# Kernel optimization log

Measured on AMD Instinct MI355X. Metric: run time of the kernel, lower is better.

The kernel has to match this reference:

```python
import jax, jax.numpy as jnp
import numpy as np

C = 128      # hidden_channels
H = 4        # heads
DH = C // H
G = 4096     # num genes (segments)
R = 4096     # num reactions
E = 65536    # total (reaction, gene) pairs
LMAX = 64    # padded segment length
NB = 4       # blocks: 2 encoder SABs + 1 PMA + 1 decoder SAB
EPS = 1e-5


def _ln(x, g, b):
    m = jnp.mean(x, axis=-1, keepdims=True)
    v = jnp.mean((x - m) ** 2, axis=-1, keepdims=True)
    return (x - m) * jax.lax.rsqrt(v + EPS) * g + b


def setup_inputs() -> dict:
    key = jax.random.key(0)
    ks = jax.random.split(key, 12)
    sc = 1.0 / np.sqrt(C)
    zb = jnp.zeros((NB, C), jnp.float32)
    ob = jnp.ones((NB, C), jnp.float32)
    # every gene gets >= 1 reaction (matches realistic GEM mapping; avoids empty segments)
    gene_idx = jnp.sort(jnp.concatenate([
        jnp.arange(G, dtype=jnp.int32),
        jax.random.randint(ks[8], (E - G,), 0, G, jnp.int32)]))
    return {
        'reaction_features': jax.random.normal(ks[0], (R, C), jnp.float32),
        'Wq': jax.random.normal(ks[1], (NB, C, C), jnp.float32) * sc,
        'Wk': jax.random.normal(ks[2], (NB, C, C), jnp.float32) * sc,
        'Wv': jax.random.normal(ks[3], (NB, C, C), jnp.float32) * sc,
        'Wo': jax.random.normal(ks[4], (NB, C, C), jnp.float32) * sc,
        'bq': zb, 'bk': zb, 'bv': zb, 'bo': zb,
        'Wlin': jax.random.normal(ks[5], (NB, C, C), jnp.float32) * sc,
        'blin': zb,
        'g1': ob, 'b1': zb, 'g2': ob, 'b2': zb,
        'seed': jax.random.normal(ks[6], (1, 1, C), jnp.float32) * sc,
        'rxn_idx': jax.random.randint(ks[7], (E,), 0, R, jnp.int32),
        'gene_idx': gene_idx,
        'num_genes': G,
        'Lmax': LMAX,
    }


def _forward(reaction_features, Wq, Wk, Wv, Wo, bq, bk, bv, bo, Wlin, blin,
             g1, b1, g2, b2, seed, rxn_idx, gene_idx, num_genes, Lmax):
    E_ = gene_idx.shape[0]
    feats = reaction_features[rxn_idx]                      # [E, C] gather
    counts = jax.ops.segment_sum(jnp.ones((E_,), jnp.int32), gene_idx,
                                 num_segments=num_genes)
    starts = jnp.cumsum(counts) - counts                    # first flat index of each segment
    pos = jnp.arange(E_, dtype=jnp.int32) - starts[gene_idx]
    # to_dense_batch: [G, Lmax, C] + mask
    x = jnp.zeros((num_genes, Lmax, C), feats.dtype).at[gene_idx, pos].set(feats, mode='drop')
    mask = jnp.zeros((num_genes, Lmax), bool).at[gene_idx, pos].set(True, mode='drop')

    def mab(q_in, kv_in, q_mask, kv_mask, i):
        B, Lq, _ = q_in.shape
        Lk = kv_in.shape[1]
        q = (q_in @ Wq[i] + bq[i]).reshape(B, Lq, H, DH)
        k = (kv_in @ Wk[i] + bk[i]).reshape(B, Lk, H, DH)
        v = (kv_in @ Wv[i] + bv[i]).reshape(B, Lk, H, DH)
        scores = jnp.einsum('bqhd,bkhd->bhqk', q, k) / np.sqrt(DH)
        if kv_mask is not None:
            scores = jnp.where(kv_mask[:, None, None, :], scores, -1e30)
        a = jax.nn.softmax(scores, axis=-1)
        attn = jnp.einsum('bhqk,bkhd->bqhd', a, v).reshape(B, Lq, C) @ Wo[i] + bo[i]
        if q_mask is not None:
            attn = jnp.where(q_mask[:, :, None], attn, 0.0)
        out = _ln(attn + q_in, g1[i], b1[i])
        out = out + jax.nn.relu(out @ Wlin[i] + blin[i])
        return _ln(out, g2[i], b2[i])

    h = mab(x, x, mask, mask, 0)          # encoder SAB 1
    h = mab(h, h, mask, mask, 1)          # encoder SAB 2
    s = jnp.broadcast_to(seed, (num_genes, seed.shape[1], C))
    h = mab(s, h, None, mask, 2)          # PMA (1 seed point)
    h = mab(h, h, None, None, 3)          # decoder SAB
    h = jnp.nan_to_num(h)
    return h.reshape(num_genes, -1)       # [G, C] (concat over 1 seed)


def reference(reaction_features, Wq, Wk, Wv, Wo, bq, bk, bv, bo, Wlin, blin,
              g1, b1, g2, b2, seed, rxn_idx, gene_idx, num_genes, Lmax):
    return _forward(reaction_features, Wq, Wk, Wv, Wo, bq, bk, bv, bo, Wlin,
                    blin, g1, b1, g2, b2, seed, rxn_idx, gene_idx, num_genes, Lmax)
```

## Files before the change

### kernel.cpp

```cpp
#include <hip/hip_runtime.h>
#include <hip/hip_bf16.h>
#include <math.h>

#define C 128
#define H 4
#define LMAX 64
#define EPS 1e-5f
#define ISQ 0.17677669529663687f

using short8  = __attribute__((ext_vector_type(8))) short;
using short4v = __attribute__((ext_vector_type(4))) short;
using f32x4   = __attribute__((ext_vector_type(4))) float;

__device__ __forceinline__ float wsum(float v){
  #pragma unroll
  for (int o = 32; o > 0; o >>= 1) v += __shfl_xor(v, o, 64);
  return v;
}
__device__ __forceinline__ float wmax(float v){
  #pragma unroll
  for (int o = 32; o > 0; o >>= 1) v = fmaxf(v, __shfl_xor(v, o, 64));
  return v;
}
__device__ __forceinline__ short f2bs(float f){
  __hip_bfloat16 b = __float2bfloat16(f);
  union { __hip_bfloat16 b; short u; } cv; cv.b = b; return cv.u;
}
__device__ __forceinline__ float b2f(short u){
  return __uint_as_float(((unsigned)(unsigned short)u) << 16);
}

__global__ void prep_wfrag(const float* __restrict__ Wq, const float* __restrict__ Wk,
                           const float* __restrict__ Wv, const float* __restrict__ Wo,
                           const float* __restrict__ Wlin, short* __restrict__ wf){
  int bid = blockIdx.x, l = threadIdx.x;
  int tile = bid & 31, mb = bid >> 5;
  int mat = mb >> 2, blk = mb & 3;
  const float* W = (mat==0?Wq : mat==1?Wk : mat==2?Wv : mat==3?Wo : Wlin) + blk*C*C;
  int nt = tile >> 2, kt = tile & 3;
  int col = nt*16 + (l & 15);
  int k0  = kt*32 + ((l >> 4) << 3);
  short8 v;
  #pragma unroll
  for (int j = 0; j < 8; j++) v[j] = f2bs(W[(k0 + j)*C + col]);
  *(short8*)(wf + ((size_t)mb*32 + tile)*512 + (size_t)l*8) = v;
}

__global__ void prep_qrow(const float* __restrict__ seed, const float* __restrict__ Wq,
                          const float* __restrict__ bq, float* __restrict__ qrow){
  int t = threadIdx.x;
  const float* wq2 = Wq + 2*C*C;
  float acc = bq[2*C + t];
  #pragma unroll 4
  for (int k = 0; k < C; k++) acc = fmaf(seed[k], wq2[k*C + t], acc);
  qrow[t] = acc;
}

__global__ void seg_kernel(const int* __restrict__ gidx, int E, int G,
                           int* __restrict__ starts, int* __restrict__ counts,
                           int* __restrict__ cnt, int* __restrict__ gcr){
  int g = blockIdx.x * blockDim.x + threadIdx.x;
  if (g >= G) return;
  int lo = 0, hi = E;
  while (lo < hi){ int m = (lo + hi) >> 1; if (gidx[m] < g) lo = m + 1; else hi = m; }
  int s = lo; hi = E;
  while (lo < hi){ int m = (lo + hi) >> 1; if (gidx[m] < g + 1) lo = m + 1; else hi = m; }
  starts[g] = s;
  int c_ = lo - s; counts[g] = c_;
  int L = c_ > LMAX ? LMAX : c_; if (L < 1) L = 1;
  int cl = (L - 1) >> 4;
  int r = atomicAdd(&cnt[cl], 1);
  gcr[g] = (cl << 28) | r;
}

__global__ void fill_kernel(int G, const int* __restrict__ cnt, const int* __restrict__ gcr,
                            int* __restrict__ binfo, int* __restrict__ nbins){
  int g = blockIdx.x * blockDim.x + threadIdx.x;
  if (g >= G) return;
  int nb1 = (cnt[0] + 3) >> 2, nb2 = (cnt[1] + 1) >> 1, nb3 = cnt[2];
  if (g == 0) *nbins = nb1 + nb2 + nb3 + cnt[3];
  int v = gcr[g]; int cl = v >> 28; int r = v & 0x0FFFFFFF;
  int bin, slot;
  if      (cl == 0){ bin = r >> 2;             slot = r & 3; }
  else if (cl == 1){ bin = nb1 + (r >> 1);     slot = (r & 1) * 2; }
  else if (cl == 2){ bin = nb1 + nb2 + r;      slot = 0; }
  else             { bin = nb1 + nb2 + nb3 + r; slot = 0; }
  binfo[bin*4 + slot] = g;
}

__device__ __forceinline__ f32x4 mfma4(short8 a0, short8 a1, short8 a2, short8 a3,
                                       const short* __restrict__ wf, int nt, int l){
  f32x4 acc = {0.f, 0.f, 0.f, 0.f};
  acc = __builtin_amdgcn_mfma_f32_16x16x32_bf16(a0, *(const short8*)(wf + ((nt*4+0)*64 + l)*8), acc, 0,0,0);
  acc = __builtin_amdgcn_mfma_f32_16x16x32_bf16(a1, *(const short8*)(wf + ((nt*4+1)*64 + l)*8), acc, 0,0,0);
  acc = __builtin_amdgcn_mfma_f32_16x16x32_bf16(a2, *(const short8*)(wf + ((nt*4+2)*64 + l)*8), acc, 0,0,0);
  acc = __builtin_amdgcn_mfma_f32_16x16x32_bf16(a3, *(const short8*)(wf + ((nt*4+3)*64 + l)*8), acc, 0,0,0);
  return acc;
}

__device__ __forceinline__ void ln_rows(const short (*src)[136], short (*dst)[136],
                                        const float* __restrict__ gg,
                                        const float* __restrict__ bb, int t){
  int row = t >> 2, q4 = t & 3;
  float v[32];
  float sm = 0.f;
  #pragma unroll
  for (int kk = 0; kk < 32; ++kk){
    float x = b2f(src[row][q4*32 + kk]);
    v[kk] = x; sm += x;
  }
  sm += __shfl_xor(sm, 1);
  sm += __shfl_xor(sm, 2);
  float mean = sm * (1.f/128.f);
  float s2 = 0.f;
  #pragma unroll
  for (int kk = 0; kk < 32; ++kk){ float d = v[kk] - mean; s2 += d*d; }
  s2 += __shfl_xor(s2, 1);
  s2 += __shfl_xor(s2, 2);
  float rs = rsqrtf(s2*(1.f/128.f) + EPS);
  #pragma unroll
  for (int kk = 0; kk < 32; ++kk){
    int col = q4*32 + kk;
    dst[row][col] = f2bs((v[kk] - mean)*rs*gg[col] + bb[col]);
  }
}

__global__ __launch_bounds__(256, 2) void gene_bin_kernel(
  const float* __restrict__ RF, const short* __restrict__ wfrag,
  const float* __restrict__ qrow,
  const float* __restrict__ bq, const float* __restrict__ bk,
  const float* __restrict__ bv, const float* __restrict__ bo,
  const float* __restrict__ blin,
  const float* __restrict__ g1, const float* __restrict__ b1,
  const float* __restrict__ g2, const float* __restrict__ b2,
  const int* __restrict__ rxn_idx, const int* __restrict__ starts,
  const int* __restrict__ counts, const int* __restrict__ binfo,
  const int* __restrict__ meta, float* __restrict__ pooled)
{
  if ((int)blockIdx.x >= meta[0]) return;
  __shared__ short xb[64][136];
  __shared__ short qb[64][136];
  __shared__ short kb[64][136];
  __shared__ short vt[128][72];
  __shared__ __align__(16) short sc[64][72];
  __shared__ float qrl[C];
  __shared__ int mg[4], mL[4], ms0[4], mbase[4];

  const int bin = blockIdx.x;
  const int t = threadIdx.x, w = t >> 6, l = t & 63;
  const int hi = l >> 4, c = l & 15;

  if (t == 0){
    int s = 0;
    while (s < 4){
      int g = binfo[bin*4 + s];
      if (g >= 0){
        int Lg = counts[g]; if (Lg > LMAX) Lg = LMAX;
        int ntg = (Lg + 15) >> 4;
        for (int u = 0; u < ntg; ++u){ mg[s+u] = g; mL[s+u] = Lg; ms0[s+u] = starts[g]; mbase[s+u] = s; }
        s += ntg;
      } else { mg[s] = -1; mL[s] = 0; ms0[s] = 0; mbase[s] = s; s++; }
    }
  }
  if (t < C) qrl[t] = qrow[t];
  __syncthreads();

  for (int idx = t; idx < 64*16; idx += 256){
    int row = idx >> 4, ch = idx & 15;
    int s = row >> 4;
    int g = mg[s];
    int ro = row - mbase[s]*16;
    short8 u = {0,0,0,0,0,0,0,0};
    if (g >= 0 && ro < mL[s]){
      int rr = rxn_idx[ms0[s] + ro];
      const float* src = RF + (size_t)rr*C + ch*8;
      float4 v0 = *(const float4*)(src);
      float4 v1 = *(const float4*)(src + 4);
      u[0]=f2bs(v0.x); u[1]=f2bs(v0.y); u[2]=f2bs(v0.z); u[3]=f2bs(v0.w);
      u[4]=f2bs(v1.x); u[5]=f2bs(v1.y); u[6]=f2bs(v1.z); u[7]=f2bs(v1.w);
    }
    *(short8*)&xb[row][ch*8] = u;
  }
  {
    short8 z = {0,0,0,0,0,0,0,0};
    for (int idx = t; idx < 64*9; idx += 256){
      int row = idx / 9, ch = idx - row*9;
      *(short8*)&sc[row][ch*8] = z;
    }
  }
  __syncthreads();

  const int myg = mg[w];

  for (int blk = 0; blk < 2; ++blk){
    {
      short8 ax[4][4];
      #pragma unroll
      for (int mt = 0; mt < 4; ++mt)
        #pragma unroll
        for (int kk = 0; kk < 4; ++kk)
          ax[mt][kk] = *(const short8*)&xb[mt*16 + c][kk*32 + hi*8];
      #pragma unroll
      for (int i = 0; i < 6; ++i){
        int pr = w + 4*i;
        int mat = pr >> 3, nt = pr & 7;
        const short* wfm = wfrag + (size_t)(mat*4 + blk)*16384;
        const float* bias = (mat == 0 ? bq : mat == 1 ? bk : bv);
        int col = nt*16 + c;
        float bb = bias[blk*C + col];
        #pragma unroll
        for (int mt = 0; mt < 4; ++mt){
          f32x4 acc = mfma4(ax[mt][0], ax[mt][1], ax[mt][2], ax[mt][3], wfm, nt, l);
          if (mat == 2){
            short4v pk;
            #pragma unroll
            for (int r = 0; r < 4; r++) pk[r] = f2bs(acc[r] + bb);
            *(short4v*)&vt[col][mt*16 + hi*4] = pk;
          } else if (mat == 0){
            #pragma unroll
            for (int r = 0; r < 4; r++) qb[mt*16 + hi*4 + r][col] = f2bs(acc[r] + bb);
          } else {
            #pragma unroll
            for (int r = 0; r < 4; r++) kb[mt*16 + hi*4 + r][col] = f2bs(acc[r] + bb);
          }
        }
      }
    }
    __syncthreads();

    for (int h = 0; h < H; ++h){
      if (myg >= 0){
        short8 a = *(const short8*)&qb[w*16 + c][h*32 + hi*8];
        #pragma unroll
        for (int kt = 0; kt < 4; ++kt){
          if (mg[kt] == myg){
            short8 b = *(const short8*)&kb[kt*16 + c][h*32 + hi*8];
            f32x4 acc = {0.f, 0.f, 0.f, 0.f};
            acc = __builtin_amdgcn_mfma_f32_16x16x32_bf16(a, b, acc, 0,0,0);
            #pragma unroll
            for (int r = 0; r < 4; r++) sc[w*16 + hi*4 + r][kt*16 + c] = f2bs(acc[r] * ISQ);
          }
        }
      }
      {
        int row = t >> 2, q4 = t & 3;
        int s = row >> 4;
        if (mg[s] >= 0){
          int kbeg = mbase[s]*16;
          int kend = kbeg + mL[s];
          int send = kbeg + (((mL[s] + 15) >> 4) << 4);
          int b0 = q4*16;
          float e[16];
          float mx = -3.4e38f;
          #pragma unroll
          for (int kk = 0; kk < 16; ++kk){
            int col = b0 + kk;
            bool ok = (col >= kbeg) && (col < kend);
            float lg = ok ? b2f(sc[row][col]) : -3.4e38f;
            e[kk] = lg;
            mx = fmaxf(mx, lg);
          }
          mx = fmaxf(mx, __shfl_xor(mx, 1));
          mx = fmaxf(mx, __shfl_xor(mx, 2));
          float sm = 0.f;
          #pragma unroll
          for (int kk = 0; kk < 16; ++kk){
            int col = b0 + kk;
            bool ok = (col >= kbeg) && (col < kend);
            float ee = ok ? __expf(e[kk] - mx) : 0.f;
            e[kk] = ee; sm += ee;
          }
          sm += __shfl_xor(sm, 1);
          sm += __shfl_xor(sm, 2);
          float inv = 1.f / sm;
          #pragma unroll
          for (int kk = 0; kk < 16; ++kk){
            int col = b0 + kk;
            if (col >= kbeg && col < send)
              sc[row][col] = f2bs((col < kend) ? e[kk]*inv : 0.f);
          }
        }
      }
      if (myg >= 0){
        #pragma unroll
        for (int dt = 0; dt < 2; ++dt){
          f32x4 acc = {0.f, 0.f, 0.f, 0.f};
          #pragma unroll
          for (int ks = 0; ks < 2; ++ks){
            short8 a = *(const short8*)&sc[w*16 + c][ks*32 + hi*8];
            short8 b = *(const short8*)&vt[h*32 + dt*16 + c][ks*32 + hi*8];
            acc = __builtin_amdgcn_mfma_f32_16x16x32_bf16(a, b, acc, 0,0,0);
          }
          int col = h*32 + dt*16 + c;
          #pragma unroll
          for (int r = 0; r < 4; r++) qb[w*16 + hi*4 + r][col] = f2bs(acc[r]);
        }
      }
    }
    __syncthreads();

    {
      short8 aq[4][4];
      #pragma unroll
      for (int mt = 0; mt < 4; ++mt)
        #pragma unroll
        for (int kk = 0; kk < 4; ++kk)
          aq[mt][kk] = *(const short8*)&qb[mt*16 + c][kk*32 + hi*8];
      const short* wfo = wfrag + (size_t)(3*4 + blk)*16384;
      #pragma unroll
      for (int i = 0; i < 2; ++i){
        int nt = w + 4*i;
        int col = nt*16 + c;
        float bb = bo[blk*C + col];
        #pragma unroll
        for (int mt = 0; mt < 4; ++mt){
          f32x4 acc = mfma4(aq[mt][0], aq[mt][1], aq[mt][2], aq[mt][3], wfo, nt, l);
          #pragma unroll
          for (int r = 0; r < 4; r++){
            int row = mt*16 + hi*4 + r;
            xb[row][col] = f2bs(acc[r] + bb + b2f(xb[row][col]));
          }
        }
      }
    }
    __syncthreads();
    ln_rows(xb, xb, g1 + blk*C, b1 + blk*C, t);
    __syncthreads();

    {
      short8 af[4][4];
      #pragma unroll
      for (int mt = 0; mt < 4; ++mt)
        #pragma unroll
        for (int kk = 0; kk < 4; ++kk)
          af[mt][kk] = *(const short8*)&xb[mt*16 + c][kk*32 + hi*8];
      const short* wfl = wfrag + (size_t)(4*4 + blk)*16384;
      #pragma unroll
      for (int i = 0; i < 2; ++i){
        int nt = w + 4*i;
        int col = nt*16 + c;
        float bb = blin[blk*C + col];
        #pragma unroll
        for (int mt = 0; mt < 4; ++mt){
          f32x4 acc = mfma4(af[mt][0], af[mt][1], af[mt][2], af[mt][3], wfl, nt, l);
          #pragma unroll
          for (int r = 0; r < 4; r++){
            int row = mt*16 + hi*4 + r;
            kb[row][col] = f2bs(b2f(xb[row][col]) + fmaxf(acc[r] + bb, 0.f));
          }
        }
      }
    }
    __syncthreads();
    ln_rows(kb, xb, g2 + blk*C, b2 + blk*C, t);
    __syncthreads();
  }

  {
    short8 ap[4][4];
    #pragma unroll
    for (int mt = 0; mt < 4; ++mt)
      #pragma unroll
      for (int kk = 0; kk < 4; ++kk)
        ap[mt][kk] = *(const short8*)&xb[mt*16 + c][kk*32 + hi*8];
    const short* wfk2 = wfrag + (size_t)(1*4 + 2)*16384;
    const short* wfv2 = wfrag + (size_t)(2*4 + 2)*16384;
    #pragma unroll
    for (int i = 0; i < 4; ++i){
      int pr = w + 4*i;
      int mat = pr >> 3, nt = pr & 7;
      const short* wfm = mat ? wfv2 : wfk2;
      const float* bias = mat ? bv : bk;
      int col = nt*16 + c;
      float bb = bias[2*C + col];
      #pragma unroll
      for (int mt = 0; mt < 4; ++mt){
        f32x4 acc = mfma4(ap[mt][0], ap[mt][1], ap[mt][2], ap[mt][3], wfm, nt, l);
        if (!mat){
          #pragma unroll
          for (int r = 0; r < 4; r++) kb[mt*16 + hi*4 + r][col] = f2bs(acc[r] + bb);
        } else {
          short4v pk;
          #pragma unroll
          for (int r = 0; r < 4; r++) pk[r] = f2bs(acc[r] + bb);
          *(short4v*)&vt[col][mt*16 + hi*4] = pk;
        }
      }
    }
  }
  __syncthreads();
  {
    int g = mg[w];
    if (g >= 0 && mbase[w] == w){
      int L = mL[w];
      int row = w*16 + l;
      float* ps = (float*)&sc[0][0];
      #pragma unroll
      for (int h = 0; h < 4; ++h){
        float a = -3.4e38f;
        if (l < L){
          float acc = 0.f;
          #pragma unroll 8
          for (int dd = 0; dd < 32; ++dd)
            acc = fmaf(b2f(kb[row][h*32 + dd]), qrl[h*32 + dd], acc);
          a = acc * ISQ;
        }
        float mx = wmax(a);
        float e = (l < L) ? __expf(a - mx) : 0.f;
        float s = wsum(e);
        ps[(w*4 + h)*64 + l] = e / s;
      }
      #pragma unroll
      for (int half = 0; half < 2; ++half){
        int d = l + half*64;
        int h = d >> 5;
        float acc = 0.f;
        for (int kk = 0; kk < L; ++kk)
          acc = fmaf(ps[(w*4 + h)*64 + kk], b2f(vt[d][w*16 + kk]), acc);
        pooled[(size_t)g*C + d] = acc;
      }
    }
  }
}

__device__ __forceinline__ void gemmf(const float (*src)[132], const float* __restrict__ W,
                                      float (&o)[4], int col, int rg){
  #pragma unroll
  for (int r = 0; r < 4; ++r) o[r] = 0.f;
  #pragma unroll 8
  for (int k = 0; k < 128; ++k){
    float wv = W[k*C + col];
    #pragma unroll
    for (int r = 0; r < 4; ++r) o[r] = fmaf(src[rg*4 + r][k], wv, o[r]);
  }
}

__device__ __forceinline__ void ln16f(float (*buf)[132], const float* __restrict__ gg,
                                      const float* __restrict__ bb, int t){
  int row = t >> 4, cg = t & 15;
  float v[8]; float s = 0.f;
  #pragma unroll
  for (int k = 0; k < 8; ++k){ v[k] = buf[row][cg*8 + k]; s += v[k]; }
  s += __shfl_xor(s,1); s += __shfl_xor(s,2); s += __shfl_xor(s,4); s += __shfl_xor(s,8);
  float mean = s * (1.f/128.f);
  float q = 0.f;
  #pragma unroll
  for (int k = 0; k < 8; ++k){ float d = v[k] - mean; q += d*d; }
  q += __shfl_xor(q,1); q += __shfl_xor(q,2); q += __shfl_xor(q,4); q += __shfl_xor(q,8);
  float rs = rsqrtf(q*(1.f/128.f) + EPS);
  #pragma unroll
  for (int k = 0; k < 8; ++k)
    buf[row][cg*8 + k] = (v[k] - mean)*rs*gg[cg*8 + k] + bb[cg*8 + k];
}

__global__ __launch_bounds__(512) void tail_kernel(
  const float* __restrict__ pooled,
  const float* __restrict__ Wv, const float* __restrict__ Wo,
  const float* __restrict__ Wlin,
  const float* __restrict__ bv, const float* __restrict__ bo,
  const float* __restrict__ blin,
  const float* __restrict__ g1, const float* __restrict__ b1,
  const float* __restrict__ g2, const float* __restrict__ b2,
  const float* __restrict__ seed, float* __restrict__ out, int G)
{
  __shared__ float ta[16][132];
  __shared__ float tb[16][132];
  const int t = threadIdx.x;
  const int g0 = blockIdx.x * 16;
  const int col = t & 127, rg = t >> 7;
  float o[4], res[4];

  if (t < 256){
    int row = t >> 4, ch = t & 15;
    float4 v0 = {0,0,0,0}, v1 = {0,0,0,0};
    if (g0 + row < G){
      const float* src = pooled + (size_t)(g0 + row)*C + ch*8;
      v0 = *(const float4*)(src);
      v1 = *(const float4*)(src + 4);
    }
    *(float4*)&ta[row][ch*8] = v0;
    *(float4*)&ta[row][ch*8 + 4] = v1;
  }
  __syncthreads();

  gemmf(ta, Wo + 2*C*C, o, col, rg);
  {
    float ss = seed[col], bb = bo[2*C + col];
    #pragma unroll
    for (int r = 0; r < 4; ++r) tb[rg*4 + r][col] = o[r] + bb + ss;
  }
  __syncthreads();
  if (t < 256) ln16f(tb, g1 + 2*C, b1 + 2*C, t);
  __syncthreads();
  gemmf(tb, Wlin + 2*C*C, o, col, rg);
  {
    float bb = blin[2*C + col];
    #pragma unroll
    for (int r = 0; r < 4; ++r) ta[rg*4 + r][col] = tb[rg*4 + r][col] + fmaxf(o[r] + bb, 0.f);
  }
  __syncthreads();
  if (t < 256) ln16f(ta, g2 + 2*C, b2 + 2*C, t);
  __syncthreads();
  gemmf(ta, Wv + 3*C*C, o, col, rg);
  {
    float bb = bv[3*C + col];
    #pragma unroll
    for (int r = 0; r < 4; ++r) tb[rg*4 + r][col] = o[r] + bb;
  }
  __syncthreads();
  gemmf(tb, Wo + 3*C*C, o, col, rg);
  {
    float bb = bo[3*C + col];
    #pragma unroll
    for (int r = 0; r < 4; ++r) res[r] = ta[rg*4 + r][col];
    #pragma unroll
    for (int r = 0; r < 4; ++r) ta[rg*4 + r][col] = o[r] + bb + res[r];
  }
  __syncthreads();
  if (t < 256) ln16f(ta, g1 + 3*C, b1 + 3*C, t);
  __syncthreads();
  gemmf(ta, Wlin + 3*C*C, o, col, rg);
  {
    float bb = blin[3*C + col];
    #pragma unroll
    for (int r = 0; r < 4; ++r) tb[rg*4 + r][col] = ta[rg*4 + r][col] + fmaxf(o[r] + bb, 0.f);
  }
  __syncthreads();
  if (t < 256) ln16f(tb, g2 + 3*C, b2 + 3*C, t);
  __syncthreads();
  for (int idx = t; idx < 16*128; idx += 512){
    int row = idx >> 7, cc = idx & 127;
    if (g0 + row < G){
      float v = tb[row][cc];
      if (isnan(v)) v = 0.f;
      else if (isinf(v)) v = v > 0 ? 3.402823466e38f : -3.402823466e38f;
      out[(size_t)(g0 + row)*C + cc] = v;
    }
  }
}

extern "C" void kernel_launch(void* const* d_in, const int* in_sizes, int n_in,
                              void* d_out, int out_size, void* d_ws, size_t ws_size,
                              hipStream_t stream){
  const float* RF   = (const float*)d_in[0];
  const float* Wq   = (const float*)d_in[1];
  const float* Wk   = (const float*)d_in[2];
  const float* Wv   = (const float*)d_in[3];
  const float* Wo   = (const float*)d_in[4];
  const float* bq   = (const float*)d_in[5];
  const float* bk   = (const float*)d_in[6];
  const float* bv   = (const float*)d_in[7];
  const float* bo   = (const float*)d_in[8];
  const float* Wlin = (const float*)d_in[9];
  const float* blin = (const float*)d_in[10];
  const float* g1   = (const float*)d_in[11];
  const float* b1   = (const float*)d_in[12];
  const float* g2   = (const float*)d_in[13];
  const float* b2   = (const float*)d_in[14];
  const float* seed = (const float*)d_in[15];
  const int* rxn    = (const int*)d_in[16];
  const int* gidx   = (const int*)d_in[17];

  int E = in_sizes[16];
  int G = out_size / C;

  char* base = (char*)d_ws;
  short* wfrag = (short*)base;
  float* qrow  = (float*)(base + 655360);
  int*   meta  = (int*)(base + 655872);
  int*   starts= (int*)(base + 655936);
  int*   counts= (int*)(base + 655936 + (size_t)4*G);
  int*   gcr   = (int*)(base + 655936 + (size_t)8*G);
  int*   binfo = (int*)(base + 655936 + (size_t)12*G);
  float* pooled= (float*)(base + 655936 + (size_t)28*G);

  hipMemsetAsync(meta, 0, 64, stream);
  hipMemsetAsync(binfo, 0xFF, (size_t)16*G, stream);
  prep_wfrag<<<640, 64, 0, stream>>>(Wq, Wk, Wv, Wo, Wlin, wfrag);
  prep_qrow<<<1, 128, 0, stream>>>(seed, Wq, bq, qrow);
  seg_kernel<<<(G + 255)/256, 256, 0, stream>>>(gidx, E, G, starts, counts, meta + 1, gcr);
  fill_kernel<<<(G + 255)/256, 256, 0, stream>>>(G, meta + 1, gcr, binfo, meta);
  gene_bin_kernel<<<G, 256, 0, stream>>>(RF, wfrag, qrow, bq, bk, bv, bo, blin,
      g1, b1, g2, b2, rxn, starts, counts, binfo, meta, pooled);
  tail_kernel<<<(G + 15)/16, 512, 0, stream>>>(pooled, Wv, Wo, Wlin, bv, bo, blin,
      g1, b1, g2, b2, seed, (float*)d_out, G);
}
```

Before: 252.3 us.

## Fold qrow prep into fill kernel, prefetch Wo/Wlin fragments, unroll tail GEMM

Removes the separate single-block prep_qrow launch by computing the seed query row inside block 0 of fill_kernel. In the gene-bin kernel it loads the Wo and Wlin MFMA B-fragments into registers before the attention loop and the output projection, so global-load latency overlaps other work. It also raises the unroll factor of the tail kernel's fp32 GEMM loop. The prefetched fragments add about 64 VGPRs of live state per thread, which may reduce occupancy.

```diff
diff --git a/kernel.cpp b/kernel.cpp
--- a/kernel.cpp
+++ b/kernel.cpp
@@ -27,7 +27,7 @@
   union { __hip_bfloat16 b; short u; } cv; cv.b = b; return cv.u;
 }
 __device__ __forceinline__ float b2f(short u){
-  return __uint_as_float(((unsigned)(unsigned short)u) << 16);
+  return __uint_as_float(((unsigned)u & 0xFFFFu) << 16);
 }
 
 __global__ void prep_wfrag(const float* __restrict__ Wq, const float* __restrict__ Wk,
@@ -44,16 +44,6 @@
   #pragma unroll
   for (int j = 0; j < 8; j++) v[j] = f2bs(W[(k0 + j)*C + col]);
   *(short8*)(wf + ((size_t)mb*32 + tile)*512 + (size_t)l*8) = v;
-}
-
-__global__ void prep_qrow(const float* __restrict__ seed, const float* __restrict__ Wq,
-                          const float* __restrict__ bq, float* __restrict__ qrow){
-  int t = threadIdx.x;
-  const float* wq2 = Wq + 2*C*C;
-  float acc = bq[2*C + t];
-  #pragma unroll 4
-  for (int k = 0; k < C; k++) acc = fmaf(seed[k], wq2[k*C + t], acc);
-  qrow[t] = acc;
 }
 
 __global__ void seg_kernel(const int* __restrict__ gidx, int E, int G,
@@ -74,7 +64,17 @@
 }
 
 __global__ void fill_kernel(int G, const int* __restrict__ cnt, const int* __restrict__ gcr,
-                            int* __restrict__ binfo, int* __restrict__ nbins){
+                            int* __restrict__ binfo, int* __restrict__ nbins,
+                            const float* __restrict__ seed, const float* __restrict__ Wq,
+                            const float* __restrict__ bq, float* __restrict__ qrow){
+  if (blockIdx.x == 0 && threadIdx.x < 128){
+    int tq = threadIdx.x;
+    const float* wq2 = Wq + 2*C*C;
+    float acc = bq[2*C + tq];
+    #pragma unroll 4
+    for (int k = 0; k < C; k++) acc = fmaf(seed[k], wq2[k*C + tq], acc);
+    qrow[tq] = acc;
+  }
   int g = blockIdx.x * blockDim.x + threadIdx.x;
   if (g >= G) return;
   int nb1 = (cnt[0] + 3) >> 2, nb2 = (cnt[1] + 1) >> 1, nb3 = cnt[2];
@@ -95,6 +95,15 @@
   acc = __builtin_amdgcn_mfma_f32_16x16x32_bf16(a1, *(const short8*)(wf + ((nt*4+1)*64 + l)*8), acc, 0,0,0);
   acc = __builtin_amdgcn_mfma_f32_16x16x32_bf16(a2, *(const short8*)(wf + ((nt*4+2)*64 + l)*8), acc, 0,0,0);
   acc = __builtin_amdgcn_mfma_f32_16x16x32_bf16(a3, *(const short8*)(wf + ((nt*4+3)*64 + l)*8), acc, 0,0,0);
+  return acc;
+}
+__device__ __forceinline__ f32x4 mfma4r(short8 a0, short8 a1, short8 a2, short8 a3,
+                                        const short8 (&bf)[4]){
+  f32x4 acc = {0.f, 0.f, 0.f, 0.f};
+  acc = __builtin_amdgcn_mfma_f32_16x16x32_bf16(a0, bf[0], acc, 0,0,0);
+  acc = __builtin_amdgcn_mfma_f32_16x16x32_bf16(a1, bf[1], acc, 0,0,0);
+  acc = __builtin_amdgcn_mfma_f32_16x16x32_bf16(a2, bf[2], acc, 0,0,0);
+  acc = __builtin_amdgcn_mfma_f32_16x16x32_bf16(a3, bf[3], acc, 0,0,0);
   return acc;
 }
 
@@ -228,6 +237,18 @@
     }
     __syncthreads();
 
+    short8 woPF[2][4];
+    {
+      const short* wfo = wfrag + (size_t)(3*4 + blk)*16384;
+      #pragma unroll
+      for (int i = 0; i < 2; ++i){
+        int nt = w + 4*i;
+        #pragma unroll
+        for (int kt = 0; kt < 4; ++kt)
+          woPF[i][kt] = *(const short8*)(wfo + ((nt*4 + kt)*64 + l)*8);
+      }
+    }
+
     for (int h = 0; h < H; ++h){
       if (myg >= 0){
         short8 a = *(const short8*)&qb[w*16 + c][h*32 + hi*8];
@@ -299,6 +320,18 @@
     }
     __syncthreads();
 
+    short8 flPF[2][4];
+    {
+      const short* wfl = wfrag + (size_t)(4*4 + blk)*16384;
+      #pragma unroll
+      for (int i = 0; i < 2; ++i){
+        int nt = w + 4*i;
+        #pragma unroll
+        for (int kt = 0; kt < 4; ++kt)
+          flPF[i][kt] = *(const short8*)(wfl + ((nt*4 + kt)*64 + l)*8);
+      }
+    }
+
     {
       short8 aq[4][4];
       #pragma unroll
@@ -306,7 +339,6 @@
         #pragma unroll
         for (int kk = 0; kk < 4; ++kk)
           aq[mt][kk] = *(const short8*)&qb[mt*16 + c][kk*32 + hi*8];
-      const short* wfo = wfrag + (size_t)(3*4 + blk)*16384;
       #pragma unroll
       for (int i = 0; i < 2; ++i){
         int nt = w + 4*i;
@@ -314,7 +346,7 @@
         float bb = bo[blk*C + col];
         #pragma unroll
         for (int mt = 0; mt < 4; ++mt){
-          f32x4 acc = mfma4(aq[mt][0], aq[mt][1], aq[mt][2], aq[mt][3], wfo, nt, l);
+          f32x4 acc = mfma4r(aq[mt][0], aq[mt][1], aq[mt][2], aq[mt][3], woPF[i]);
           #pragma unroll
           for (int r = 0; r < 4; r++){
             int row = mt*16 + hi*4 + r;
@@ -334,7 +366,6 @@
         #pragma unroll
         for (int kk = 0; kk < 4; ++kk)
           af[mt][kk] = *(const short8*)&xb[mt*16 + c][kk*32 + hi*8];
-      const short* wfl = wfrag + (size_t)(4*4 + blk)*16384;
       #pragma unroll
       for (int i = 0; i < 2; ++i){
         int nt = w + 4*i;
@@ -342,7 +373,7 @@
         float bb = blin[blk*C + col];
         #pragma unroll
         for (int mt = 0; mt < 4; ++mt){
-          f32x4 acc = mfma4(af[mt][0], af[mt][1], af[mt][2], af[mt][3], wfl, nt, l);
+          f32x4 acc = mfma4r(af[mt][0], af[mt][1], af[mt][2], af[mt][3], flPF[i]);
           #pragma unroll
           for (int r = 0; r < 4; r++){
             int row = mt*16 + hi*4 + r;
@@ -427,7 +458,7 @@
                                       float (&o)[4], int col, int rg){
   #pragma unroll
   for (int r = 0; r < 4; ++r) o[r] = 0.f;
-  #pragma unroll 8
+  #pragma unroll 32
   for (int k = 0; k < 128; ++k){
     float wv = W[k*C + col];
     #pragma unroll
@@ -577,9 +608,9 @@
   hipMemsetAsync(meta, 0, 64, stream);
   hipMemsetAsync(binfo, 0xFF, (size_t)16*G, stream);
   prep_wfrag<<<640, 64, 0, stream>>>(Wq, Wk, Wv, Wo, Wlin, wfrag);
-  prep_qrow<<<1, 128, 0, stream>>>(seed, Wq, bq, qrow);
   seg_kernel<<<(G + 255)/256, 256, 0, stream>>>(gidx, E, G, starts, counts, meta + 1, gcr);
-  fill_kernel<<<(G + 255)/256, 256, 0, stream>>>(G, meta + 1, gcr, binfo, meta);
+  fill_kernel<<<(G + 255)/256, 256, 0, stream>>>(G, meta + 1, gcr, binfo, meta,
+      seed, Wq, bq, qrow);
   gene_bin_kernel<<<G, 256, 0, stream>>>(RF, wfrag, qrow, bq, bk, bv, bo, blin,
       g1, b1, g2, b2, rxn, starts, counts, binfo, meta, pooled);
   tail_kernel<<<(G + 15)/16, 512, 0, stream>>>(pooled, Wv, Wo, Wlin, bv, bo, blin,
```

After: 260.1 us. +3.1%, slower.
